# Performance work log

Hardware: AMD Instinct MI355X
Metric: run time of the kernel (lower is better)

The kernel has to match this reference:

```python
import jax, jax.numpy as jnp
import numpy as np

N_NODES = 100000
N_EDGES = 1000000
N_RELS = 8
N_HEADS = 4
IN_FEAT = 64
OUT_FEAT = 64
D_HEAD = OUT_FEAT // N_HEADS
LEAKY_SLOPE = 0.2


def setup_inputs() -> dict:
    key = jax.random.key(0)
    ks = jax.random.split(key, 8)
    x = jax.random.normal(ks[0], (N_NODES, IN_FEAT), dtype=jnp.float32)
    src_idx = jax.random.randint(ks[1], (N_EDGES,), 0, N_NODES)
    dst_idx = jax.random.randint(ks[2], (N_EDGES,), 0, N_NODES)
    edge_rel = jnp.sort(jax.random.randint(ks[3], (N_EDGES,), 0, N_RELS))
    # xavier-ish small init for weights
    conv_weights = jax.random.normal(ks[4], (N_RELS, N_HEADS, IN_FEAT, D_HEAD), dtype=jnp.float32) * 0.1
    attn_l = jax.random.normal(ks[5], (N_RELS, N_HEADS, D_HEAD), dtype=jnp.float32) * 0.1
    attn_r = jax.random.normal(ks[6], (N_RELS, N_HEADS, D_HEAD), dtype=jnp.float32) * 0.1
    h_bias = jnp.zeros((OUT_FEAT,), dtype=jnp.float32)
    return {
        'x': x, 'src_idx': src_idx, 'dst_idx': dst_idx, 'edge_rel': edge_rel,
        'conv_weights': conv_weights, 'attn_l': attn_l, 'attn_r': attn_r,
        'h_bias': h_bias,
    }


def reference(x, src_idx, dst_idx, edge_rel, conv_weights, attn_l, attn_r, h_bias):
    N = x.shape[0]
    # Per-relation transform of all node features: [R, N, H, D]
    feat_all = jnp.einsum('ni,rhid->rnhd', x, conv_weights)
    # Per-relation attention logits per node: [R, N, H]
    el_all = jnp.einsum('rnhd,rhd->rnh', feat_all, attn_l)
    er_all = jnp.einsum('rnhd,rhd->rnh', feat_all, attn_r)
    # Gather per-edge quantities (relation-specific transform of src/dst)
    feat_e = feat_all[edge_rel, src_idx]          # [E, H, D]
    el = el_all[edge_rel, src_idx]                # [E, H]
    er = er_all[edge_rel, dst_idx]                # [E, H]
    s = jax.nn.leaky_relu(el + er, negative_slope=LEAKY_SLOPE)
    # Edge softmax over incoming edges of each destination node (per head)
    m = jax.ops.segment_max(s, dst_idx, num_segments=N)      # [N, H]
    e = jnp.exp(s - m[dst_idx])                               # [E, H]
    denom = jax.ops.segment_sum(e, dst_idx, num_segments=N)   # [N, H]
    w = e / jnp.maximum(denom[dst_idx], jnp.float32(1e-16))   # [E, H]
    # Weighted aggregation of source features into destination nodes
    agg = jax.ops.segment_sum(feat_e * w[..., None], dst_idx, num_segments=N)  # [N, H, D]
    h = agg.reshape(N, OUT_FEAT) + h_bias
    # activation=None, dropout in eval mode -> identity
    return h
```

## Files before the change

### kernel.cpp

```cpp
#include <hip/hip_runtime.h>
#include <hip/hip_bf16.h>

#define NN 100000
#define NE 1000000
#define NR 8

#define EB 1024
#define NBLK 977
#define NBUCK 196
#define NT (NBUCK*NBLK)
#define NBB 749

#define CAP 224

typedef unsigned short u16;
typedef unsigned int u32;
typedef __attribute__((ext_vector_type(8))) short bf16x8;
typedef __attribute__((ext_vector_type(4))) float f32x4;

static __device__ __forceinline__ float bf2f(u16 u) {
    union { u32 i; float f; } v; v.i = ((u32)u) << 16; return v.f;
}
static __device__ __forceinline__ float bflo(u32 u) {
    union { u32 i; float f; } v; v.i = u << 16; return v.f;
}
static __device__ __forceinline__ float bfhi(u32 u) {
    union { u32 i; float f; } v; v.i = u & 0xffff0000u; return v.f;
}
static __device__ __forceinline__ u16 f2bf(float f) {
    __hip_bfloat16 h = __float2bfloat16(f);
    return *reinterpret_cast<u16*>(&h);
}
static __device__ __forceinline__ float ldf(const void* p, int idx, int isf32) {
    return isf32 ? ((const float*)p)[idx] : bf2f(((const u16*)p)[idx]);
}

static __device__ __forceinline__ int detect_wave(const u16* xw, int lane)
{
    int insane = 0;
    for (int k = lane; k < 512; k += 64) {
        u16 w = xw[k];
        int ex = (w >> 7) & 0xFF;
        bool sane = ((w & 0x7FFF) == 0) || (ex >= 96 && ex <= 159);
        insane += sane ? 0 : 1;
    }
    for (int off = 32; off; off >>= 1) insane += __shfl_down(insane, off);
    return insane;
}

__global__ __launch_bounds__(256) void k_cvt(const void* __restrict__ xin,
                                             u16* __restrict__ xb, int* __restrict__ flag)
{
    __shared__ int sflag;
    int t = threadIdx.x;
    if (t < 64) {
        int insane = detect_wave((const u16*)xin, t);
        if (t == 0) {
            sflag = (insane > 50) ? 1 : 0;
            if (blockIdx.x == 0) *flag = sflag;
        }
    }
    __syncthreads();
    int isf32 = sflag;
    int i = blockIdx.x * 256 + t;
    if (i >= NN * 8) return;
    if (isf32) {
        const float* xf = (const float*)xin;
        u16 o[8];
#pragma unroll
        for (int j = 0; j < 8; ++j) o[j] = f2bf(xf[i * 8 + j]);
        uint4 v;
        v.x = (u32)o[0] | ((u32)o[1] << 16);
        v.y = (u32)o[2] | ((u32)o[3] << 16);
        v.z = (u32)o[4] | ((u32)o[5] << 16);
        v.w = (u32)o[6] | ((u32)o[7] << 16);
        ((uint4*)xb)[i] = v;
    } else {
        ((uint4*)xb)[i] = ((const uint4*)xin)[i];
    }
}

__global__ __launch_bounds__(256) void k0_prep(const void* __restrict__ xin,
                        const void* __restrict__ cw, const void* __restrict__ al,
                        const void* __restrict__ ar, u16* __restrict__ Bpre)
{
    __shared__ int sflag;
    int t = threadIdx.x;
    if (t < 64) {
        int insane = detect_wave((const u16*)xin, t);
        if (t == 0) sflag = (insane > 50) ? 1 : 0;
    }
    __syncthreads();
    int isf32 = sflag;
    int tid = blockIdx.x * 256 + t;
    if (tid >= NR * 5120) return;
    int r = tid / 5120, rem = tid % 5120;
    int c = rem >> 3, j = rem & 7;
    int nt = c >> 7, kk = (c >> 6) & 1, lc = c & 63;
    int i = kk * 32 + ((lc >> 4) << 3) + j;
    int d = lc & 15;
    u16 val;
    if (nt < 4) {
        val = f2bf(ldf(cw, ((r * 4 + nt) * 64 + i) * 16 + d, isf32));
    } else if (d < 8) {
        int h = d >> 1;
        const void* attn = (d & 1) ? ar : al;
        float s = 0.f;
        for (int dd = 0; dd < 16; ++dd)
            s += ldf(cw, ((r * 4 + h) * 64 + i) * 16 + dd, isf32)
               * ldf(attn, (r * 4 + h) * 16 + dd, isf32);
        val = f2bf(s);
    } else {
        val = 0;
    }
    Bpre[tid] = val;
}

__global__ __launch_bounds__(256) void k1_feat(
    const u16* __restrict__ xb, const u16* __restrict__ Bpre,
    u16* __restrict__ feat_all, float* __restrict__ el_all, float* __restrict__ er_all)
{
    __shared__ alignas(16) u16 ldsA[4096];
    __shared__ alignas(16) u16 ldsB[5120];
    __shared__ alignas(16) u16 ldsF[4096];
    int n0 = blockIdx.x * 64;
    int tid = threadIdx.x;
    int wave = tid >> 6, lane = tid & 63;
    int col = lane & 15, quad = lane >> 4;

    for (int c = tid; c < 512; c += 256) {
        int mt = c >> 7, kk = (c >> 6) & 1, lc = c & 63;
        int node = n0 + mt * 16 + (lc & 15);
        if (node >= NN) node = NN - 1;
        int kbase = kk * 32 + ((lc >> 4) << 3);
        *(uint4*)&ldsA[c * 8] = *(const uint4*)&xb[node * 64 + kbase];
    }
    __syncthreads();
    bf16x8 afrag0 = *(bf16x8*)&ldsA[((wave * 2 + 0) * 64 + lane) * 8];
    bf16x8 afrag1 = *(bf16x8*)&ldsA[((wave * 2 + 1) * 64 + lane) * 8];

    for (int r = 0; r < NR; ++r) {
        for (int c = tid; c < 640; c += 256)
            *(uint4*)&ldsB[c * 8] = *(const uint4*)&Bpre[r * 5120 + c * 8];
        __syncthreads();

        f32x4 acc[5];
#pragma unroll
        for (int nt = 0; nt < 5; ++nt) acc[nt] = f32x4{0.f, 0.f, 0.f, 0.f};
#pragma unroll
        for (int nt = 0; nt < 5; ++nt) {
            bf16x8 b0 = *(bf16x8*)&ldsB[((nt * 2 + 0) * 64 + lane) * 8];
            bf16x8 b1 = *(bf16x8*)&ldsB[((nt * 2 + 1) * 64 + lane) * 8];
            acc[nt] = __builtin_amdgcn_mfma_f32_16x16x32_bf16(afrag0, b0, acc[nt], 0, 0, 0);
            acc[nt] = __builtin_amdgcn_mfma_f32_16x16x32_bf16(afrag1, b1, acc[nt], 0, 0, 0);
        }

        if (col < 8) {
            int h = col >> 1;
            float* dstp = (col & 1) ? er_all : el_all;
#pragma unroll
            for (int reg = 0; reg < 4; ++reg) {
                int node = n0 + wave * 16 + quad * 4 + reg;
                if (node < NN) dstp[(r * NN + node) * 4 + h] = acc[4][reg];
            }
        }
#pragma unroll
        for (int nt = 0; nt < 4; ++nt) {
            int cg = nt * 16 + col;
#pragma unroll
            for (int reg = 0; reg < 4; ++reg) {
                int row = quad * 4 + reg;
                ldsF[(wave * 16 + row) * 64 + cg] = f2bf(acc[nt][reg]);
            }
        }
        __syncthreads();
        for (int c = tid; c < 512; c += 256) {
            int nl = c >> 3, part = c & 7;
            int node = n0 + nl;
            if (node < NN)
                *(uint4*)&feat_all[(r * NN + node) * 64 + part * 8] = *(uint4*)&ldsF[c * 8];
        }
    }
}

__global__ __launch_bounds__(256) void k_binA(const int* __restrict__ dsti,
                                              int* __restrict__ histT)
{
    __shared__ int hist[NBUCK];
    int t = threadIdx.x, blk = blockIdx.x;
    if (t < NBUCK) hist[t] = 0;
    __syncthreads();
    int base = blk * EB;
    for (int j = 0; j < EB; j += 256) {
        int e = base + j + t;
        if (e < NE) atomicAdd(&hist[dsti[e] >> 9], 1);
    }
    __syncthreads();
    if (t < NBUCK) histT[t * NBLK + blk] = hist[t];
}

__global__ __launch_bounds__(256) void k_scanB1(int* __restrict__ histT,
                                                int* __restrict__ bsum)
{
    __shared__ int wtot[4];
    int t = threadIdx.x;
    int gi = blockIdx.x * 256 + t;
    int v = (gi < NT) ? histT[gi] : 0;
    int lane = t & 63, w = t >> 6;
    int s = v;
#pragma unroll
    for (int m = 1; m < 64; m <<= 1) {
        int u = __shfl_up(s, m);
        if (lane >= m) s += u;
    }
    if (lane == 63) wtot[w] = s;
    __syncthreads();
    int wb = 0;
    for (int i = 0; i < w; ++i) wb += wtot[i];
    if (gi < NT) histT[gi] = wb + s - v;
    if (t == 255) bsum[blockIdx.x] = wb + s;
}

__global__ __launch_bounds__(1024) void k_scanB2(const int* __restrict__ bsum,
                                                 int* __restrict__ boff)
{
    __shared__ int wtot[16];
    int t = threadIdx.x;
    int v = (t < NBB) ? bsum[t] : 0;
    int lane = t & 63, w = t >> 6;
    int s = v;
#pragma unroll
    for (int m = 1; m < 64; m <<= 1) {
        int u = __shfl_up(s, m);
        if (lane >= m) s += u;
    }
    if (lane == 63) wtot[w] = s;
    __syncthreads();
    int wb = 0;
    for (int i = 0; i < w; ++i) wb += wtot[i];
    if (t < NBB) boff[t] = wb + s - v;
}

__global__ __launch_bounds__(256) void k_scanB3(const int* __restrict__ boff,
                                                int* __restrict__ histT,
                                                int* __restrict__ bstart)
{
    int gi = blockIdx.x * 256 + threadIdx.x;
    if (gi < NT) {
        int val = histT[gi] + boff[blockIdx.x];
        histT[gi] = val;
        if (gi % NBLK == 0) bstart[gi / NBLK] = val;
    }
    if (gi == 0) bstart[NBUCK] = NE;
}

__global__ __launch_bounds__(256) void k_binC(
    const int* __restrict__ srci, const int* __restrict__ dsti,
    const int* __restrict__ reli, const int* __restrict__ histT,
    int* __restrict__ key_b)
{
    __shared__ int cur[NBUCK];
    int t = threadIdx.x, blk = blockIdx.x;
    if (t < NBUCK) cur[t] = histT[t * NBLK + blk];
    __syncthreads();
    int base = blk * EB;
    for (int j = 0; j < EB; j += 256) {
        int e = base + j + t;
        if (e < NE) {
            int d = dsti[e];
            int key = ((d & 511) << 20) | (reli[e] << 17) | srci[e];
            int pos = atomicAdd(&cur[d >> 9], 1);
            key_b[pos] = key;
        }
    }
}

__global__ __launch_bounds__(1024) void k_binD(
    const int* __restrict__ bstart, const int* __restrict__ key_b,
    int* __restrict__ key_s, int* __restrict__ off)
{
    __shared__ int cnt[512];
    __shared__ int wtot[8];
    int t = threadIdx.x, b = blockIdx.x;
    int s0 = bstart[b], s1 = bstart[b + 1];
    if (t < 512) cnt[t] = 0;
    __syncthreads();
    for (int j = s0 + t; j < s1; j += 1024)
        atomicAdd(&cnt[(key_b[j] >> 20) & 511], 1);
    __syncthreads();
    int excl = 0;
    if (t < 512) {
        int v = cnt[t];
        int lane = t & 63, w = t >> 6;
        int s = v;
#pragma unroll
        for (int m = 1; m < 64; m <<= 1) {
            int u = __shfl_up(s, m);
            if (lane >= m) s += u;
        }
        if (lane == 63) wtot[w] = s;
        __syncthreads();
        int wb = 0;
        for (int i = 0; i < w; ++i) wb += wtot[i];
        excl = s0 + wb + s - v;
        int d = (b << 9) + t;
        if (d < NN) off[d] = excl;
    } else {
        __syncthreads();
    }
    __syncthreads();
    if (t < 512) cnt[t] = excl;
    if (b == 0 && t == 0) off[NN] = NE;
    __syncthreads();
    for (int j = s0 + t; j < s1; j += 1024) {
        int key = key_b[j];
        int pos = atomicAdd(&cnt[(key >> 20) & 511], 1);
        key_s[pos] = key;
    }
}

__global__ __launch_bounds__(256) void k3_node(
    const int* __restrict__ off, const int* __restrict__ key_s,
    const float* __restrict__ el_all, const float* __restrict__ er_all,
    const u16* __restrict__ feat_all, const void* __restrict__ bias,
    const int* __restrict__ flag, void* __restrict__ out)
{
    __shared__ int   ldsOffs[65];
    __shared__ int   ldsKey[4][CAP];
    __shared__ float ldsEE[4][CAP][4];
    int t = threadIdx.x;
    int wave = t >> 6, lane = t & 63;
    int eg = lane >> 4;
    int fl = lane & 15;
    int h  = fl >> 2;
    int d0 = blockIdx.x * 64;
    int isf32 = *flag;

    if (t < 65) ldsOffs[t] = off[min(d0 + t, NN)];
    __syncthreads();

    int dlo = wave * 16;
    int estart = ldsOffs[dlo], eend = ldsOffs[dlo + 16];
    int count = eend - estart;
    int scount = min(count, CAP);

    for (int j = lane; j < scount; j += 64) {
        int key = key_s[estart + j];
        int rel = (key >> 17) & 7, src = key & 131071;
        int d = d0 + ((key >> 20) & 63);
        int kk = rel * NN + src;
        f32x4 el = *(const f32x4*)&el_all[kk * 4];
        f32x4 er = *(const f32x4*)&er_all[(rel * NN + d) * 4];
        f32x4 ee;
#pragma unroll
        for (int q = 0; q < 4; ++q) {
            float v = el[q] + er[q];
            v = v > 0.f ? v : 0.2f * v;
            ee[q] = __expf(v);
        }
        ldsKey[wave][j] = kk;
        *(f32x4*)&ldsEE[wave][j][0] = ee;
    }

    float bv0 = ldf(bias, fl * 4 + 0, isf32);
    float bv1 = ldf(bias, fl * 4 + 1, isf32);
    float bv2 = ldf(bias, fl * 4 + 2, isf32);
    float bv3 = ldf(bias, fl * 4 + 3, isf32);

    for (int nl = 0; nl < 16; ++nl) {
        int d = d0 + dlo + nl;
        if (d >= NN) break;
        int s  = ldsOffs[dlo + nl] - estart;
        int e1 = ldsOffs[dlo + nl + 1] - estart;
        float acc0 = 0.f, acc1 = 0.f, acc2 = 0.f, acc3 = 0.f, accW = 0.f;

        int e1c = min(e1, CAP);
        for (int base = s; base < e1c; base += 16) {
            int kk[4]; float w[4];
#pragma unroll
            for (int q = 0; q < 4; ++q) {
                int idx = base + q * 4 + eg;
                bool vld = idx < e1c;
                kk[q] = vld ? ldsKey[wave][idx] : 0;
                w[q]  = vld ? ldsEE[wave][idx][h] : 0.f;
            }
            uint2 u[4];
#pragma unroll
            for (int q = 0; q < 4; ++q)
                u[q] = *(const uint2*)&feat_all[kk[q] * 64 + fl * 4];
#pragma unroll
            for (int q = 0; q < 4; ++q) {
                acc0 += bflo(u[q].x) * w[q];
                acc1 += bfhi(u[q].x) * w[q];
                acc2 += bflo(u[q].y) * w[q];
                acc3 += bfhi(u[q].y) * w[q];
                accW += w[q];
            }
        }
        for (int base = max(s, CAP); base < e1; base += 4) {
            int idx = base + eg;
            int kk0 = 0; float w0 = 0.f;
            if (idx < e1) {
                int key = key_s[estart + idx];
                int rel = (key >> 17) & 7, src = key & 131071;
                kk0 = rel * NN + src;
                float v = el_all[kk0 * 4 + h] + er_all[(rel * NN + d) * 4 + h];
                v = v > 0.f ? v : 0.2f * v;
                w0 = __expf(v);
            }
            uint2 u = *(const uint2*)&feat_all[kk0 * 64 + fl * 4];
            acc0 += bflo(u.x) * w0;
            acc1 += bfhi(u.x) * w0;
            acc2 += bflo(u.y) * w0;
            acc3 += bfhi(u.y) * w0;
            accW += w0;
        }

#pragma unroll
        for (int m = 16; m < 64; m <<= 1) {
            acc0 += __shfl_xor(acc0, m);
            acc1 += __shfl_xor(acc1, m);
            acc2 += __shfl_xor(acc2, m);
            acc3 += __shfl_xor(acc3, m);
            accW += __shfl_xor(accW, m);
        }
        float invh = 1.f / fmaxf(accW, 1e-16f);
        if (eg == 0) {
            float o0 = acc0 * invh + bv0;
            float o1 = acc1 * invh + bv1;
            float o2 = acc2 * invh + bv2;
            float o3 = acc3 * invh + bv3;
            if (isf32) {
                ((f32x4*)out)[d * 16 + fl] = f32x4{o0, o1, o2, o3};
            } else {
                uint2 st;
                st.x = (u32)f2bf(o0) | ((u32)f2bf(o1) << 16);
                st.y = (u32)f2bf(o2) | ((u32)f2bf(o3) << 16);
                *(uint2*)&((u16*)out)[d * 64 + fl * 4] = st;
            }
        }
    }
}

extern "C" void kernel_launch(void* const* d_in, const int* in_sizes, int n_in,
                              void* d_out, int out_size, void* d_ws, size_t ws_size,
                              hipStream_t stream)
{
    const void* x   = d_in[0];
    const int* srci = (const int*)d_in[1];
    const int* dsti = (const int*)d_in[2];
    const int* reli = (const int*)d_in[3];
    const void* cw  = d_in[4];
    const void* al  = d_in[5];
    const void* ar  = d_in[6];
    const void* hb  = d_in[7];

    char* ws = (char*)d_ws;
    u16*   feat_all = (u16*)  (ws + 0);
    float* el_all   = (float*)(ws + 102400000);
    float* er_all   = (float*)(ws + 115200000);
    int*   key_s    = (int*)  (ws + 128000000);
    int*   key_b    = (int*)  (ws + 132000000);
    int*   off      = (int*)  (ws + 136000000);
    int*   histT    = (int*)  (ws + 136400064);
    int*   bsum     = (int*)  (ws + 137166032);
    int*   boff     = (int*)  (ws + 137169040);
    int*   bstart   = (int*)  (ws + 137172048);
    u16*   Bpre     = (u16*)  (ws + 137172880);
    u16*   xb       = (u16*)  (ws + 137254800);
    int*   flag     = (int*)  (ws + 150054800);

    k_cvt<<<(NN * 8 + 255) / 256, 256, 0, stream>>>(x, xb, flag);
    k0_prep<<<(NR * 5120 + 255) / 256, 256, 0, stream>>>(x, cw, al, ar, Bpre);
    k1_feat<<<(NN + 63) / 64, 256, 0, stream>>>(xb, Bpre, feat_all, el_all, er_all);
    k_binA<<<NBLK, 256, 0, stream>>>(dsti, histT);
    k_scanB1<<<NBB, 256, 0, stream>>>(histT, bsum);
    k_scanB2<<<1, 1024, 0, stream>>>(bsum, boff);
    k_scanB3<<<NBB, 256, 0, stream>>>(boff, histT, bstart);
    k_binC<<<NBLK, 256, 0, stream>>>(srci, dsti, reli, histT, key_b);
    k_binD<<<NBUCK, 1024, 0, stream>>>(bstart, key_b, key_s, off);
    k3_node<<<(NN + 63) / 64, 256, 0, stream>>>(off, key_s, el_all, er_all, feat_all,
                                                hb, flag, d_out);
}
```

Baseline: 219.9 us.

## Merge prep kernels, fold scan pass, drop LDS B staging, retile node aggregation

Three independent preprocessing kernels (x conversion, weight prep, destination histogram) are merged into one launch with block-range dispatch, and the third scan pass is folded into the second scan and the binning kernel, cutting two launches. The feature GEMM now reads B fragments straight from global memory instead of staging them in LDS with a barrier, and double-buffers the output tile. The node aggregation kernel is remapped so each lane group owns one destination with 8 features via 16-byte loads, processing edges serially, removing cross-lane shuffle reductions. This trades fewer launches and syncs for less edge-level parallelism per node and possible load imbalance.

```diff
diff --git a/kernel.cpp b/kernel.cpp
--- a/kernel.cpp
+++ b/kernel.cpp
@@ -12,6 +12,10 @@
 #define NBB 749
 
 #define CAP 224
+
+#define CVT_BLKS 3125
+#define K0_BLKS  160
+#define PRE_BLKS (CVT_BLKS + K0_BLKS + NBLK)
 
 typedef unsigned short u16;
 typedef unsigned int u32;
@@ -48,72 +52,84 @@
     return insane;
 }
 
-__global__ __launch_bounds__(256) void k_cvt(const void* __restrict__ xin,
-                                             u16* __restrict__ xb, int* __restrict__ flag)
+__global__ __launch_bounds__(256) void k_pre(
+    const void* __restrict__ xin, u16* __restrict__ xb, int* __restrict__ flag,
+    const void* __restrict__ cw, const void* __restrict__ al,
+    const void* __restrict__ ar, u16* __restrict__ Bpre,
+    const int* __restrict__ dsti, int* __restrict__ histT)
 {
     __shared__ int sflag;
+    __shared__ int hist[NBUCK];
     int t = threadIdx.x;
-    if (t < 64) {
-        int insane = detect_wave((const u16*)xin, t);
-        if (t == 0) {
-            sflag = (insane > 50) ? 1 : 0;
-            if (blockIdx.x == 0) *flag = sflag;
-        }
-    }
-    __syncthreads();
-    int isf32 = sflag;
-    int i = blockIdx.x * 256 + t;
-    if (i >= NN * 8) return;
-    if (isf32) {
-        const float* xf = (const float*)xin;
-        u16 o[8];
-#pragma unroll
-        for (int j = 0; j < 8; ++j) o[j] = f2bf(xf[i * 8 + j]);
-        uint4 v;
-        v.x = (u32)o[0] | ((u32)o[1] << 16);
-        v.y = (u32)o[2] | ((u32)o[3] << 16);
-        v.z = (u32)o[4] | ((u32)o[5] << 16);
-        v.w = (u32)o[6] | ((u32)o[7] << 16);
-        ((uint4*)xb)[i] = v;
+    int b = blockIdx.x;
+
+    if (b < CVT_BLKS) {
+        if (t < 64) {
+            int insane = detect_wave((const u16*)xin, t);
+            if (t == 0) {
+                sflag = (insane > 50) ? 1 : 0;
+                if (b == 0) *flag = sflag;
+            }
+        }
+        __syncthreads();
+        int isf32 = sflag;
+        int i = b * 256 + t;
+        if (i >= NN * 8) return;
+        if (isf32) {
+            const float* xf = (const float*)xin;
+            u16 o[8];
+#pragma unroll
+            for (int j = 0; j < 8; ++j) o[j] = f2bf(xf[i * 8 + j]);
+            uint4 v;
+            v.x = (u32)o[0] | ((u32)o[1] << 16);
+            v.y = (u32)o[2] | ((u32)o[3] << 16);
+            v.z = (u32)o[4] | ((u32)o[5] << 16);
+            v.w = (u32)o[6] | ((u32)o[7] << 16);
+            ((uint4*)xb)[i] = v;
+        } else {
+            ((uint4*)xb)[i] = ((const uint4*)xin)[i];
+        }
+    } else if (b < CVT_BLKS + K0_BLKS) {
+        if (t < 64) {
+            int insane = detect_wave((const u16*)xin, t);
+            if (t == 0) sflag = (insane > 50) ? 1 : 0;
+        }
+        __syncthreads();
+        int isf32 = sflag;
+        int tid = (b - CVT_BLKS) * 256 + t;
+        if (tid >= NR * 5120) return;
+        int r = tid / 5120, rem = tid % 5120;
+        int c = rem >> 3, j = rem & 7;
+        int nt = c >> 7, kk = (c >> 6) & 1, lc = c & 63;
+        int i = kk * 32 + ((lc >> 4) << 3) + j;
+        int d = lc & 15;
+        u16 val;
+        if (nt < 4) {
+            val = f2bf(ldf(cw, ((r * 4 + nt) * 64 + i) * 16 + d, isf32));
+        } else if (d < 8) {
+            int h = d >> 1;
+            const void* attn = (d & 1) ? ar : al;
+            float s = 0.f;
+            for (int dd = 0; dd < 16; ++dd)
+                s += ldf(cw, ((r * 4 + h) * 64 + i) * 16 + dd, isf32)
+                   * ldf(attn, (r * 4 + h) * 16 + dd, isf32);
+            val = f2bf(s);
+        } else {
+            val = 0;
+        }
+        Bpre[tid] = val;
     } else {
-        ((uint4*)xb)[i] = ((const uint4*)xin)[i];
-    }
-}
-
-__global__ __launch_bounds__(256) void k0_prep(const void* __restrict__ xin,
-                        const void* __restrict__ cw, const void* __restrict__ al,
-                        const void* __restrict__ ar, u16* __restrict__ Bpre)
-{
-    __shared__ int sflag;
-    int t = threadIdx.x;
-    if (t < 64) {
-        int insane = detect_wave((const u16*)xin, t);
-        if (t == 0) sflag = (insane > 50) ? 1 : 0;
-    }
-    __syncthreads();
-    int isf32 = sflag;
-    int tid = blockIdx.x * 256 + t;
-    if (tid >= NR * 5120) return;
-    int r = tid / 5120, rem = tid % 5120;
-    int c = rem >> 3, j = rem & 7;
-    int nt = c >> 7, kk = (c >> 6) & 1, lc = c & 63;
-    int i = kk * 32 + ((lc >> 4) << 3) + j;
-    int d = lc & 15;
-    u16 val;
-    if (nt < 4) {
-        val = f2bf(ldf(cw, ((r * 4 + nt) * 64 + i) * 16 + d, isf32));
-    } else if (d < 8) {
-        int h = d >> 1;
-        const void* attn = (d & 1) ? ar : al;
-        float s = 0.f;
-        for (int dd = 0; dd < 16; ++dd)
-            s += ldf(cw, ((r * 4 + h) * 64 + i) * 16 + dd, isf32)
-               * ldf(attn, (r * 4 + h) * 16 + dd, isf32);
-        val = f2bf(s);
-    } else {
-        val = 0;
-    }
-    Bpre[tid] = val;
+        int blk = b - CVT_BLKS - K0_BLKS;
+        if (t < NBUCK) hist[t] = 0;
+        __syncthreads();
+        int base = blk * EB;
+        for (int j = 0; j < EB; j += 256) {
+            int e = base + j + t;
+            if (e < NE) atomicAdd(&hist[dsti[e] >> 9], 1);
+        }
+        __syncthreads();
+        if (t < NBUCK) histT[t * NBLK + blk] = hist[t];
+    }
 }
 
 __global__ __launch_bounds__(256) void k1_feat(
@@ -121,8 +137,7 @@
     u16* __restrict__ feat_all, float* __restrict__ el_all, float* __restrict__ er_all)
 {
     __shared__ alignas(16) u16 ldsA[4096];
-    __shared__ alignas(16) u16 ldsB[5120];
-    __shared__ alignas(16) u16 ldsF[4096];
+    __shared__ alignas(16) u16 ldsF[2][4096];
     int n0 = blockIdx.x * 64;
     int tid = threadIdx.x;
     int wave = tid >> 6, lane = tid & 63;
@@ -140,17 +155,14 @@
     bf16x8 afrag1 = *(bf16x8*)&ldsA[((wave * 2 + 1) * 64 + lane) * 8];
 
     for (int r = 0; r < NR; ++r) {
-        for (int c = tid; c < 640; c += 256)
-            *(uint4*)&ldsB[c * 8] = *(const uint4*)&Bpre[r * 5120 + c * 8];
-        __syncthreads();
-
+        int buf = r & 1;
         f32x4 acc[5];
 #pragma unroll
         for (int nt = 0; nt < 5; ++nt) acc[nt] = f32x4{0.f, 0.f, 0.f, 0.f};
 #pragma unroll
         for (int nt = 0; nt < 5; ++nt) {
-            bf16x8 b0 = *(bf16x8*)&ldsB[((nt * 2 + 0) * 64 + lane) * 8];
-            bf16x8 b1 = *(bf16x8*)&ldsB[((nt * 2 + 1) * 64 + lane) * 8];
+            bf16x8 b0 = *(const bf16x8*)&Bpre[r * 5120 + ((nt * 2 + 0) * 64 + lane) * 8];
+            bf16x8 b1 = *(const bf16x8*)&Bpre[r * 5120 + ((nt * 2 + 1) * 64 + lane) * 8];
             acc[nt] = __builtin_amdgcn_mfma_f32_16x16x32_bf16(afrag0, b0, acc[nt], 0, 0, 0);
             acc[nt] = __builtin_amdgcn_mfma_f32_16x16x32_bf16(afrag1, b1, acc[nt], 0, 0, 0);
         }
@@ -170,7 +182,7 @@
 #pragma unroll
             for (int reg = 0; reg < 4; ++reg) {
                 int row = quad * 4 + reg;
-                ldsF[(wave * 16 + row) * 64 + cg] = f2bf(acc[nt][reg]);
+                ldsF[buf][(wave * 16 + row) * 64 + cg] = f2bf(acc[nt][reg]);
             }
         }
         __syncthreads();
@@ -178,25 +190,9 @@
             int nl = c >> 3, part = c & 7;
             int node = n0 + nl;
             if (node < NN)
-                *(uint4*)&feat_all[(r * NN + node) * 64 + part * 8] = *(uint4*)&ldsF[c * 8];
-        }
-    }
-}
-
-__global__ __launch_bounds__(256) void k_binA(const int* __restrict__ dsti,
-                                              int* __restrict__ histT)
-{
-    __shared__ int hist[NBUCK];
-    int t = threadIdx.x, blk = blockIdx.x;
-    if (t < NBUCK) hist[t] = 0;
-    __syncthreads();
-    int base = blk * EB;
-    for (int j = 0; j < EB; j += 256) {
-        int e = base + j + t;
-        if (e < NE) atomicAdd(&hist[dsti[e] >> 9], 1);
-    }
-    __syncthreads();
-    if (t < NBUCK) histT[t * NBLK + blk] = hist[t];
+                *(uint4*)&feat_all[(r * NN + node) * 64 + part * 8] = *(uint4*)&ldsF[buf][c * 8];
+        }
+    }
 }
 
 __global__ __launch_bounds__(256) void k_scanB1(int* __restrict__ histT,
@@ -222,9 +218,12 @@
 }
 
 __global__ __launch_bounds__(1024) void k_scanB2(const int* __restrict__ bsum,
-                                                 int* __restrict__ boff)
+                                                 int* __restrict__ boff,
+                                                 const int* __restrict__ histT,
+                                                 int* __restrict__ bstart)
 {
     __shared__ int wtot[16];
+    __shared__ int sboff[NBB];
     int t = threadIdx.x;
     int v = (t < NBB) ? bsum[t] : 0;
     int lane = t & 63, w = t >> 6;
@@ -238,30 +237,30 @@
     __syncthreads();
     int wb = 0;
     for (int i = 0; i < w; ++i) wb += wtot[i];
-    if (t < NBB) boff[t] = wb + s - v;
-}
-
-__global__ __launch_bounds__(256) void k_scanB3(const int* __restrict__ boff,
-                                                int* __restrict__ histT,
-                                                int* __restrict__ bstart)
-{
-    int gi = blockIdx.x * 256 + threadIdx.x;
-    if (gi < NT) {
-        int val = histT[gi] + boff[blockIdx.x];
-        histT[gi] = val;
-        if (gi % NBLK == 0) bstart[gi / NBLK] = val;
-    }
-    if (gi == 0) bstart[NBUCK] = NE;
+    if (t < NBB) {
+        int val = wb + s - v;
+        boff[t] = val;
+        sboff[t] = val;
+    }
+    __syncthreads();
+    if (t < NBUCK) {
+        int gi = t * NBLK;
+        bstart[t] = histT[gi] + sboff[gi >> 8];
+    }
+    if (t == 0) bstart[NBUCK] = NE;
 }
 
 __global__ __launch_bounds__(256) void k_binC(
     const int* __restrict__ srci, const int* __restrict__ dsti,
     const int* __restrict__ reli, const int* __restrict__ histT,
-    int* __restrict__ key_b)
+    const int* __restrict__ boff, int* __restrict__ key_b)
 {
     __shared__ int cur[NBUCK];
     int t = threadIdx.x, blk = blockIdx.x;
-    if (t < NBUCK) cur[t] = histT[t * NBLK + blk];
+    if (t < NBUCK) {
+        int gi = t * NBLK + blk;
+        cur[t] = histT[gi] + boff[gi >> 8];
+    }
     __syncthreads();
     int base = blk * EB;
     for (int j = 0; j < EB; j += 256) {
@@ -330,9 +329,9 @@
     __shared__ float ldsEE[4][CAP][4];
     int t = threadIdx.x;
     int wave = t >> 6, lane = t & 63;
-    int eg = lane >> 4;
-    int fl = lane & 15;
-    int h  = fl >> 2;
+    int dg = lane >> 3;
+    int fl = lane & 7;
+    int h  = fl >> 1;
     int d0 = blockIdx.x * 64;
     int isf32 = *flag;
 
@@ -341,8 +340,7 @@
 
     int dlo = wave * 16;
     int estart = ldsOffs[dlo], eend = ldsOffs[dlo + 16];
-    int count = eend - estart;
-    int scount = min(count, CAP);
+    int scount = min(eend - estart, CAP);
 
     for (int j = lane; j < scount; j += 64) {
         int key = key_s[estart + j];
@@ -362,81 +360,80 @@
         *(f32x4*)&ldsEE[wave][j][0] = ee;
     }
 
-    float bv0 = ldf(bias, fl * 4 + 0, isf32);
-    float bv1 = ldf(bias, fl * 4 + 1, isf32);
-    float bv2 = ldf(bias, fl * 4 + 2, isf32);
-    float bv3 = ldf(bias, fl * 4 + 3, isf32);
-
-    for (int nl = 0; nl < 16; ++nl) {
+    float bv[8];
+#pragma unroll
+    for (int q = 0; q < 8; ++q) bv[q] = ldf(bias, fl * 8 + q, isf32);
+
+#pragma unroll
+    for (int i = 0; i < 2; ++i) {
+        int nl = i * 8 + dg;
         int d = d0 + dlo + nl;
-        if (d >= NN) break;
         int s  = ldsOffs[dlo + nl] - estart;
         int e1 = ldsOffs[dlo + nl + 1] - estart;
-        float acc0 = 0.f, acc1 = 0.f, acc2 = 0.f, acc3 = 0.f, accW = 0.f;
+        float acc[8] = {0.f, 0.f, 0.f, 0.f, 0.f, 0.f, 0.f, 0.f};
+        float accW = 0.f;
 
         int e1c = min(e1, CAP);
-        for (int base = s; base < e1c; base += 16) {
+        for (int base = s; base < e1c; base += 4) {
             int kk[4]; float w[4];
 #pragma unroll
             for (int q = 0; q < 4; ++q) {
-                int idx = base + q * 4 + eg;
+                int idx = base + q;
                 bool vld = idx < e1c;
                 kk[q] = vld ? ldsKey[wave][idx] : 0;
                 w[q]  = vld ? ldsEE[wave][idx][h] : 0.f;
             }
-            uint2 u[4];
+            uint4 u[4];
 #pragma unroll
             for (int q = 0; q < 4; ++q)
-                u[q] = *(const uint2*)&feat_all[kk[q] * 64 + fl * 4];
+                u[q] = *(const uint4*)&feat_all[kk[q] * 64 + fl * 8];
 #pragma unroll
             for (int q = 0; q < 4; ++q) {
-                acc0 += bflo(u[q].x) * w[q];
-                acc1 += bfhi(u[q].x) * w[q];
-                acc2 += bflo(u[q].y) * w[q];
-                acc3 += bfhi(u[q].y) * w[q];
+                acc[0] += bflo(u[q].x) * w[q];
+                acc[1] += bfhi(u[q].x) * w[q];
+                acc[2] += bflo(u[q].y) * w[q];
+                acc[3] += bfhi(u[q].y) * w[q];
+                acc[4] += bflo(u[q].z) * w[q];
+                acc[5] += bfhi(u[q].z) * w[q];
+                acc[6] += bflo(u[q].w) * w[q];
+                acc[7] += bfhi(u[q].w) * w[q];
                 accW += w[q];
             }
         }
-        for (int base = max(s, CAP); base < e1; base += 4) {
-            int idx = base + eg;
-            int kk0 = 0; float w0 = 0.f;
-            if (idx < e1) {
-                int key = key_s[estart + idx];
-                int rel = (key >> 17) & 7, src = key & 131071;
-                kk0 = rel * NN + src;
-                float v = el_all[kk0 * 4 + h] + er_all[(rel * NN + d) * 4 + h];
-                v = v > 0.f ? v : 0.2f * v;
-                w0 = __expf(v);
-            }
-            uint2 u = *(const uint2*)&feat_all[kk0 * 64 + fl * 4];
-            acc0 += bflo(u.x) * w0;
-            acc1 += bfhi(u.x) * w0;
-            acc2 += bflo(u.y) * w0;
-            acc3 += bfhi(u.y) * w0;
+        for (int j = max(s, CAP); j < e1; ++j) {
+            int key = key_s[estart + j];
+            int rel = (key >> 17) & 7, src = key & 131071;
+            int kk0 = rel * NN + src;
+            float v = el_all[kk0 * 4 + h] + er_all[(rel * NN + d) * 4 + h];
+            v = v > 0.f ? v : 0.2f * v;
+            float w0 = __expf(v);
+            uint4 u = *(const uint4*)&feat_all[kk0 * 64 + fl * 8];
+            acc[0] += bflo(u.x) * w0;
+            acc[1] += bfhi(u.x) * w0;
+            acc[2] += bflo(u.y) * w0;
+            acc[3] += bfhi(u.y) * w0;
+            acc[4] += bflo(u.z) * w0;
+            acc[5] += bfhi(u.z) * w0;
+            acc[6] += bflo(u.w) * w0;
+            acc[7] += bfhi(u.w) * w0;
             accW += w0;
         }
 
-#pragma unroll
-        for (int m = 16; m < 64; m <<= 1) {
-            acc0 += __shfl_xor(acc0, m);
-            acc1 += __shfl_xor(acc1, m);
-            acc2 += __shfl_xor(acc2, m);
-            acc3 += __shfl_xor(acc3, m);
-            accW += __shfl_xor(accW, m);
-        }
-        float invh = 1.f / fmaxf(accW, 1e-16f);
-        if (eg == 0) {
-            float o0 = acc0 * invh + bv0;
-            float o1 = acc1 * invh + bv1;
-            float o2 = acc2 * invh + bv2;
-            float o3 = acc3 * invh + bv3;
+        if (d < NN) {
+            float invh = 1.f / fmaxf(accW, 1e-16f);
+            float o[8];
+#pragma unroll
+            for (int q = 0; q < 8; ++q) o[q] = acc[q] * invh + bv[q];
             if (isf32) {
-                ((f32x4*)out)[d * 16 + fl] = f32x4{o0, o1, o2, o3};
+                ((f32x4*)out)[d * 16 + fl * 2]     = f32x4{o[0], o[1], o[2], o[3]};
+                ((f32x4*)out)[d * 16 + fl * 2 + 1] = f32x4{o[4], o[5], o[6], o[7]};
             } else {
-                uint2 st;
-                st.x = (u32)f2bf(o0) | ((u32)f2bf(o1) << 16);
-                st.y = (u32)f2bf(o2) | ((u32)f2bf(o3) << 16);
-                *(uint2*)&((u16*)out)[d * 64 + fl * 4] = st;
+                uint4 st;
+                st.x = (u32)f2bf(o[0]) | ((u32)f2bf(o[1]) << 16);
+                st.y = (u32)f2bf(o[2]) | ((u32)f2bf(o[3]) << 16);
+                st.z = (u32)f2bf(o[4]) | ((u32)f2bf(o[5]) << 16);
+                st.w = (u32)f2bf(o[6]) | ((u32)f2bf(o[7]) << 16);
+                *(uint4*)&((u16*)out)[d * 64 + fl * 8] = st;
             }
         }
     }
@@ -470,14 +467,11 @@
     u16*   xb       = (u16*)  (ws + 137254800);
     int*   flag     = (int*)  (ws + 150054800);
 
-    k_cvt<<<(NN * 8 + 255) / 256, 256, 0, stream>>>(x, xb, flag);
-    k0_prep<<<(NR * 5120 + 255) / 256, 256, 0, stream>>>(x, cw, al, ar, Bpre);
+    k_pre<<<PRE_BLKS, 256, 0, stream>>>(x, xb, flag, cw, al, ar, Bpre, dsti, histT);
     k1_feat<<<(NN + 63) / 64, 256, 0, stream>>>(xb, Bpre, feat_all, el_all, er_all);
-    k_binA<<<NBLK, 256, 0, stream>>>(dsti, histT);
     k_scanB1<<<NBB, 256, 0, stream>>>(histT, bsum);
-    k_scanB2<<<1, 1024, 0, stream>>>(bsum, boff);
-    k_scanB3<<<NBB, 256, 0, stream>>>(boff, histT, bstart);
-    k_binC<<<NBLK, 256, 0, stream>>>(srci, dsti, reli, histT, key_b);
+    k_scanB2<<<1, 1024, 0, stream>>>(bsum, boff, histT, bstart);
+    k_binC<<<NBLK, 256, 0, stream>>>(srci, dsti, reli, histT, boff, key_b);
     k_binD<<<NBUCK, 1024, 0, stream>>>(bstart, key_b, key_s, off);
     k3_node<<<(NN + 63) / 64, 256, 0, stream>>>(off, key_s, el_all, er_all, feat_all,
                                                 hb, flag, d_out);
```

Result: faster. 210.0 us (-4.5%).
